# Kernel optimization log

Hardware: AMD Instinct MI355X
Metric: run time of the kernel (lower is better)

## Reference

```python
import jax, jax.numpy as jnp
import numpy as np

K, D, N, W, OUT = 16, 2, 16384, 256, 1
TW = 0.2  # fixed_transition_width


def setup_inputs() -> dict:
    key = jax.random.key(0)
    ks = jax.random.split(key, 9)
    # 4x4 grid of subdomains over [0,1]^2
    edges = np.linspace(0.0, 1.0, 5).astype(np.float32)
    mins = np.array([[edges[i], edges[j]] for i in range(4) for j in range(4)], np.float32)
    maxs = mins + 0.25

    def init_w(k, shape, fan_in):
        return jax.random.normal(k, shape, jnp.float32) / np.sqrt(fan_in).astype(np.float32)

    return {
        "x": jax.random.uniform(ks[0], (N, D), jnp.float32),
        "W0": init_w(ks[1], (K, D, W), D),
        "b0": jnp.zeros((K, W), jnp.float32),
        "W1": init_w(ks[2], (K, W, W), W),
        "b1": jnp.zeros((K, W), jnp.float32),
        "W2": init_w(ks[3], (K, W, W), W),
        "b2": jnp.zeros((K, W), jnp.float32),
        "W3": init_w(ks[4], (K, W, OUT), W),
        "b3": jnp.zeros((K, OUT), jnp.float32),
        "xmins": jnp.asarray(mins),
        "xmaxs": jnp.asarray(maxs),
    }


def _cosine_window(xmins, xmaxs, wmin, x):
    """Normalized cosine partition-of-unity weights. x:[N,D], xmins/xmaxs:[K,D] -> [N,K]."""
    # smooth ramp 0->1 over [xmin-w, xmin+w] and 1->0 over [xmax-w, xmax+w], per dim
    t_l = jnp.clip((x[None] - (xmins - wmin)[:, None]) / (2.0 * wmin), 0.0, 1.0)  # [K,N,D]
    t_r = jnp.clip(((xmaxs + wmin)[:, None] - x[None]) / (2.0 * wmin), 0.0, 1.0)
    w_raw = jnp.prod(0.25 * (1.0 - jnp.cos(jnp.pi * t_l)) * (1.0 - jnp.cos(jnp.pi * t_r)), axis=-1)  # [K,N]
    w = w_raw / (jnp.sum(w_raw, axis=0, keepdims=True) + 1e-9)
    return w.T  # [N,K]


def reference(x, W0, b0, W1, b1, W2, b2, W3, b3, xmins, xmaxs):
    all_w = _cosine_window(xmins, xmaxs, TW, x)  # [N,K]
    # per-subdomain normalization of x to [-1,1]
    center = (xmins + xmaxs) * 0.5
    scale = jnp.maximum((xmaxs - xmins) * 0.5, 1e-9)
    xn = (x[None] - center[:, None]) / scale[:, None]  # [K,N,D]
    # batched small MLPs (one per subdomain), tanh hidden activations
    h = jnp.tanh(jnp.einsum('knd,kdw->knw', xn, W0) + b0[:, None])
    h = jnp.tanh(jnp.einsum('knw,kwv->knv', h, W1) + b1[:, None])
    h = jnp.tanh(jnp.einsum('knw,kwv->knv', h, W2) + b2[:, None])
    sub = jnp.einsum('knw,kwo->kno', h, W3) + b3[:, None]  # [K,N,OUT]
    # window-weighted combine; ansatz is identity in the NN output
    return jnp.einsum('nk,kno->no', all_w, sub)  # [N,OUT]
```

## Files before the change

kernel.cpp:

```cpp
#include <hip/hip_runtime.h>
#include <stdint.h>

#define TWF 0.2f
#define NPTS 16384

typedef __attribute__((ext_vector_type(8))) short short8;
typedef __attribute__((ext_vector_type(4))) float floatx4;

__device__ __forceinline__ short f2bf(float f){
  unsigned u = __float_as_uint(f);
  u += 0x7fff + ((u >> 16) & 1);
  return (short)(u >> 16);
}
__device__ __forceinline__ float bf2f(short s){
  return __uint_as_float(((unsigned)(unsigned short)s) << 16);
}
__device__ __forceinline__ float fast_tanh(float x){
  float e = __builtin_amdgcn_exp2f(x * 2.885390082f);
  float r = __builtin_amdgcn_rcpf(e + 1.f);
  return fmaf(-2.f, r, 1.f);
}
__device__ __forceinline__ float cospi_t(float t){
  return __builtin_amdgcn_cosf(t * 0.5f);
}
__device__ __forceinline__ int swz(int m, int j){
  return m * 256 + ((((j >> 3) ^ (m & 7)) << 3) | (j & 7));
}

#define WS_W      0
#define WS_CNT    (4u<<20)
#define WS_ILIST  ((4u<<20) + 4096u)
#define WS_WLIST  ((5u<<20) + 4096u)
#define CNT(k)    counts[(k) * 32]

__global__ __launch_bounds__(256) void prep_fused(
    const float* __restrict__ W1, const float* __restrict__ W2,
    const float* __restrict__ x,  const float* __restrict__ xmins,
    const float* __restrict__ xmaxs, short* __restrict__ dst,
    int* __restrict__ counts, int* __restrict__ ilist, float* __restrict__ wlist,
    float* __restrict__ out){
  if (blockIdx.x < 1024){
    int gid = blockIdx.x * 256 + threadIdx.x;
    int lane = gid & 63; int rest = gid >> 6;
    int jt = rest & 15; rest >>= 4;
    int ks = rest & 7;  rest >>= 3;
    int k  = rest & 15; int mat = rest >> 4;
    const float* W = mat ? W2 : W1;
    int j   = jt * 16 + (lane & 15);
    int kk0 = ks * 32 + (lane >> 4) * 8;
    short8 v;
    #pragma unroll
    for (int jj = 0; jj < 8; jj++)
      v[jj] = f2bf(W[k * 65536 + (kk0 + jj) * 256 + j]);
    *(short8*)(dst + (size_t)gid * 8) = v;
  } else {
    __shared__ int s_wcnt[4];
    __shared__ int s_base;
    int gid  = (blockIdx.x - 1024) * 256 + threadIdx.x;
    int t    = threadIdx.x;
    int lane = t & 63, wave = t >> 6;
    out[gid] = 0.f;
    float px = x[gid * 2 + 0], py = x[gid * 2 + 1];
    float wr[16]; float sum = 0.f;
    #pragma unroll
    for (int k = 0; k < 16; k++){
      float w = 1.f;
      #pragma unroll
      for (int d = 0; d < 2; d++){
        float xv = d ? py : px;
        float mn = xmins[k * 2 + d], mx = xmaxs[k * 2 + d];
        float tl = fminf(fmaxf((xv - (mn - TWF)) * (1.f / (2.f * TWF)), 0.f), 1.f);
        float tr = fminf(fmaxf(((mx + TWF) - xv) * (1.f / (2.f * TWF)), 0.f), 1.f);
        w *= 0.25f * (1.f - cospi_t(tl)) * (1.f - cospi_t(tr));
      }
      wr[k] = w; sum += w;
    }
    float inv = 1.f / (sum + 1e-9f);
    #pragma unroll 1
    for (int kk = 0; kk < 16; kk++){
      int k = (kk + blockIdx.x) & 15;
      bool act = wr[k] > 0.f;
      unsigned long long mask = __ballot(act);
      if (lane == 0) s_wcnt[wave] = (int)__popcll(mask);
      __syncthreads();
      int tot = s_wcnt[0] + s_wcnt[1] + s_wcnt[2] + s_wcnt[3];
      int wpre = 0;
      #pragma unroll
      for (int w = 0; w < 4; w++) wpre += (w < wave) ? s_wcnt[w] : 0;
      if (t == 0) s_base = atomicAdd(&CNT(k), tot);
      __syncthreads();
      if (act){
        int pos = s_base + wpre + (int)__popcll(mask & ((1ull << lane) - 1ull));
        ilist[k * NPTS + pos] = gid;
        wlist[k * NPTS + pos] = wr[k] * inv;
      }
    }
  }
}

__global__ __launch_bounds__(256, 3) void fbpinn_main(
    const float* __restrict__ x,  const float* __restrict__ W0, const float* __restrict__ b0,
    const float* __restrict__ b1, const float* __restrict__ b2,
    const float* __restrict__ W3, const float* __restrict__ b3,
    const float* __restrict__ xmins, const float* __restrict__ xmaxs,
    const short* __restrict__ wsw, const int* __restrict__ counts,
    const int* __restrict__ ilist, const float* __restrict__ wlist,
    float* __restrict__ out)
{
  __shared__ short lds_h[64 * 256];
  __shared__ float s_xn[64 * 2];
  __shared__ float s_win[64];
  __shared__ int   s_pidx[64];
  __shared__ float s_w3[256];
  __shared__ float s_w0[512];

  const int t    = threadIdx.x;
  const int lane = t & 63;
  const int wave = t >> 6;
  const int col  = lane & 15;
  const int quad = lane >> 4;

  int tb[17]; tb[0] = 0;
  #pragma unroll
  for (int kk = 0; kk < 16; kk++) tb[kk + 1] = tb[kk] + ((CNT(kk) + 63) >> 6);
  const int total = tb[16];

  for (int tile = blockIdx.x; tile < total; tile += gridDim.x){
    int k = 0;
    #pragma unroll
    for (int kk = 1; kk < 16; kk++) k += (tile >= tb[kk]);
    const int base = (tile - tb[k]) * 64;
    const int cnt  = CNT(k);

    __syncthreads();

    s_w3[t] = W3[k * 256 + t];
    s_w0[t] = W0[k * 512 + t];
    s_w0[256 + t] = W0[k * 512 + 256 + t];
    if (t < 64){
      int gi = base + t;
      bool valid = gi < cnt;
      int pidx = valid ? ilist[k * NPTS + gi] : 0;
      float w  = valid ? wlist[k * NPTS + gi] : 0.f;
      s_pidx[t] = pidx;
      s_win[t]  = w;
      float px = x[pidx * 2 + 0], py = x[pidx * 2 + 1];
      float cx = (xmins[k * 2 + 0] + xmaxs[k * 2 + 0]) * 0.5f;
      float cy = (xmins[k * 2 + 1] + xmaxs[k * 2 + 1]) * 0.5f;
      float sx = fmaxf((xmaxs[k * 2 + 0] - xmins[k * 2 + 0]) * 0.5f, 1e-9f);
      float sy = fmaxf((xmaxs[k * 2 + 1] - xmins[k * 2 + 1]) * 0.5f, 1e-9f);
      s_xn[t * 2 + 0] = (px - cx) / sx;
      s_xn[t * 2 + 1] = (py - cy) / sy;
    }
    __syncthreads();

    {
      short8 bfr[4], afr[4];
      #pragma unroll
      for (int jtl = 0; jtl < 4; jtl++){
        int j = (wave * 4 + jtl) * 16 + col;
        short8 b;
        #pragma unroll
        for (int i = 0; i < 8; i++) b[i] = 0;
        b[0] = (quad == 0) ? f2bf(s_w0[j])       : (short)0;
        b[1] = (quad == 0) ? f2bf(s_w0[256 + j]) : (short)0;
        bfr[jtl] = b;
      }
      #pragma unroll
      for (int mt = 0; mt < 4; mt++){
        int m = mt * 16 + col;
        short8 a;
        #pragma unroll
        for (int i = 0; i < 8; i++) a[i] = 0;
        a[0] = (quad == 0) ? f2bf(s_xn[m * 2 + 0]) : (short)0;
        a[1] = (quad == 0) ? f2bf(s_xn[m * 2 + 1]) : (short)0;
        afr[mt] = a;
      }
      floatx4 acc[4][4];
      #pragma unroll
      for (int a = 0; a < 4; a++)
        #pragma unroll
        for (int b = 0; b < 4; b++)
          acc[a][b] = (floatx4){0.f, 0.f, 0.f, 0.f};
      #pragma unroll
      for (int mt = 0; mt < 4; mt++)
        #pragma unroll
        for (int jtl = 0; jtl < 4; jtl++)
          acc[mt][jtl] = __builtin_amdgcn_mfma_f32_16x16x32_bf16(afr[mt], bfr[jtl], acc[mt][jtl], 0, 0, 0);
      #pragma unroll
      for (int jtl = 0; jtl < 4; jtl++){
        int j = (wave * 4 + jtl) * 16 + col;
        float bb = b0[k * 256 + j];
        #pragma unroll
        for (int mt = 0; mt < 4; mt++){
          #pragma unroll
          for (int r = 0; r < 4; r++){
            int m = mt * 16 + quad * 4 + r;
            lds_h[swz(m, j)] = f2bf(fast_tanh(acc[mt][jtl][r] + bb));
          }
        }
      }
      __syncthreads();
    }

    #pragma unroll 1
    for (int layer = 0; layer < 2; layer++){
      const short8* wb = (const short8*)(wsw + (size_t)layer * 1048576)
                         + ((size_t)(k * 8) * 16 + wave * 4) * 64 + lane;
      const float*  bp = layer ? b2 : b1;
      floatx4 acc[4][4];
      #pragma unroll
      for (int a = 0; a < 4; a++)
        #pragma unroll
        for (int b = 0; b < 4; b++)
          acc[a][b] = (floatx4){0.f, 0.f, 0.f, 0.f};

      short8 bcur[4];
      #pragma unroll
      for (int jtl = 0; jtl < 4; jtl++) bcur[jtl] = wb[jtl * 64];

      #pragma unroll
      for (int ks = 0; ks < 8; ks++){
        short8 bnxt[4];
        if (ks < 7){
          #pragma unroll
          for (int jtl = 0; jtl < 4; jtl++)
            bnxt[jtl] = wb[(ks + 1) * 1024 + jtl * 64];
        }
        short8 afr[4];
        #pragma unroll
        for (int mt = 0; mt < 4; mt++){
          int m   = mt * 16 + col;
          int pos = (ks * 4 + quad) ^ (m & 7);
          afr[mt] = *(const short8*)&lds_h[m * 256 + pos * 8];
        }
        #pragma unroll
        for (int mt = 0; mt < 4; mt++)
          #pragma unroll
          for (int jtl = 0; jtl < 4; jtl++)
            acc[mt][jtl] = __builtin_amdgcn_mfma_f32_16x16x32_bf16(afr[mt], bcur[jtl], acc[mt][jtl], 0, 0, 0);
        if (ks < 7){
          #pragma unroll
          for (int jtl = 0; jtl < 4; jtl++) bcur[jtl] = bnxt[jtl];
        }
      }
      __syncthreads();

      #pragma unroll
      for (int jtl = 0; jtl < 4; jtl++){
        int j = (wave * 4 + jtl) * 16 + col;
        float bb = bp[k * 256 + j];
        #pragma unroll
        for (int mt = 0; mt < 4; mt++){
          #pragma unroll
          for (int r = 0; r < 4; r++){
            int m = mt * 16 + quad * 4 + r;
            lds_h[swz(m, j)] = f2bf(fast_tanh(acc[mt][jtl][r] + bb));
          }
        }
      }
      __syncthreads();
    }

    {
      int m = t >> 2, q = t & 3;
      float dot = 0.f;
      #pragma unroll
      for (int cc = 0; cc < 8; cc++){
        int ci  = q * 8 + cc;
        int pos = ci ^ (m & 7);
        short8 hv = *(const short8*)&lds_h[m * 256 + pos * 8];
        #pragma unroll
        for (int jj = 0; jj < 8; jj++)
          dot = fmaf(bf2f(hv[jj]), s_w3[ci * 8 + jj], dot);
      }
      dot += __shfl_xor(dot, 1);
      dot += __shfl_xor(dot, 2);
      if (q == 0 && s_win[m] != 0.f)
        atomicAdd(&out[s_pidx[m]], s_win[m] * (dot + b3[k]));
    }
  }
}

extern "C" void kernel_launch(void* const* d_in, const int* in_sizes, int n_in,
                              void* d_out, int out_size, void* d_ws, size_t ws_size,
                              hipStream_t stream){
  const float* x     = (const float*)d_in[0];
  const float* W0    = (const float*)d_in[1];
  const float* b0    = (const float*)d_in[2];
  const float* W1    = (const float*)d_in[3];
  const float* b1    = (const float*)d_in[4];
  const float* W2    = (const float*)d_in[5];
  const float* b2    = (const float*)d_in[6];
  const float* W3    = (const float*)d_in[7];
  const float* b3    = (const float*)d_in[8];
  const float* xmins = (const float*)d_in[9];
  const float* xmaxs = (const float*)d_in[10];
  float* out = (float*)d_out;

  char* ws = (char*)d_ws;
  short* wsw   = (short*)(ws + WS_W);
  int*   cnts  = (int*)  (ws + WS_CNT);
  int*   ilist = (int*)  (ws + WS_ILIST);
  float* wlist = (float*)(ws + WS_WLIST);

  (void)hipMemsetAsync(cnts, 0, 4096, stream);
  prep_fused<<<1024 + NPTS / 256, 256, 0, stream>>>(W1, W2, x, xmins, xmaxs,
                                                    wsw, cnts, ilist, wlist, out);
  fbpinn_main<<<640, 256, 0, stream>>>(x, W0, b0, b1, b2, W3, b3, xmins, xmaxs,
                                       wsw, cnts, ilist, wlist, out);
}
```

Baseline: 155.3 us.

## Replace global atomic compaction with per-wave segment counts and prefix-scan lookup

The binning step no longer uses block barriers and a global atomicAdd per subdomain. Each wave now writes its compacted points into a fixed 64-slot segment and records a byte count per segment. The main kernel rebuilds per-subdomain totals and each tile's gather indices from those counts with wave shuffle reductions, a prefix scan and a binary search. This also drops the memset launch, raises the occupancy hint to 4 and enlarges the main grid to 1024 blocks, at the cost of extra scan work in every tile.

```diff
diff --git a/kernel.cpp b/kernel.cpp
--- a/kernel.cpp
+++ b/kernel.cpp
@@ -31,14 +31,13 @@
 #define WS_CNT    (4u<<20)
 #define WS_ILIST  ((4u<<20) + 4096u)
 #define WS_WLIST  ((5u<<20) + 4096u)
-#define CNT(k)    counts[(k) * 32]
 
 __global__ __launch_bounds__(256) void prep_fused(
     const float* __restrict__ W1, const float* __restrict__ W2,
     const float* __restrict__ x,  const float* __restrict__ xmins,
     const float* __restrict__ xmaxs, short* __restrict__ dst,
-    int* __restrict__ counts, int* __restrict__ ilist, float* __restrict__ wlist,
-    float* __restrict__ out){
+    unsigned char* __restrict__ cnt8, int* __restrict__ ilist,
+    float* __restrict__ wlist, float* __restrict__ out){
   if (blockIdx.x < 1024){
     int gid = blockIdx.x * 256 + threadIdx.x;
     int lane = gid & 63; int rest = gid >> 6;
@@ -54,13 +53,13 @@
       v[jj] = f2bf(W[k * 65536 + (kk0 + jj) * 256 + j]);
     *(short8*)(dst + (size_t)gid * 8) = v;
   } else {
-    __shared__ int s_wcnt[4];
-    __shared__ int s_base;
-    int gid  = (blockIdx.x - 1024) * 256 + threadIdx.x;
+    int bb   = blockIdx.x - 1024;
     int t    = threadIdx.x;
     int lane = t & 63, wave = t >> 6;
-    out[gid] = 0.f;
-    float px = x[gid * 2 + 0], py = x[gid * 2 + 1];
+    out[bb * 256 + t] = 0.f;
+    int seg = bb * 4 + wave;
+    int pt  = seg * 64 + lane;
+    float px = x[pt * 2 + 0], py = x[pt * 2 + 1];
     float wr[16]; float sum = 0.f;
     #pragma unroll
     for (int k = 0; k < 16; k++){
@@ -77,33 +76,25 @@
     }
     float inv = 1.f / (sum + 1e-9f);
     #pragma unroll 1
-    for (int kk = 0; kk < 16; kk++){
-      int k = (kk + blockIdx.x) & 15;
+    for (int k = 0; k < 16; k++){
       bool act = wr[k] > 0.f;
       unsigned long long mask = __ballot(act);
-      if (lane == 0) s_wcnt[wave] = (int)__popcll(mask);
-      __syncthreads();
-      int tot = s_wcnt[0] + s_wcnt[1] + s_wcnt[2] + s_wcnt[3];
-      int wpre = 0;
-      #pragma unroll
-      for (int w = 0; w < 4; w++) wpre += (w < wave) ? s_wcnt[w] : 0;
-      if (t == 0) s_base = atomicAdd(&CNT(k), tot);
-      __syncthreads();
+      if (lane == 0) cnt8[k * 256 + seg] = (unsigned char)__popcll(mask);
       if (act){
-        int pos = s_base + wpre + (int)__popcll(mask & ((1ull << lane) - 1ull));
-        ilist[k * NPTS + pos] = gid;
-        wlist[k * NPTS + pos] = wr[k] * inv;
+        int pos = (int)__popcll(mask & ((1ull << lane) - 1ull));
+        ilist[k * NPTS + seg * 64 + pos] = pt;
+        wlist[k * NPTS + seg * 64 + pos] = wr[k] * inv;
       }
     }
   }
 }
 
-__global__ __launch_bounds__(256, 3) void fbpinn_main(
+__global__ __launch_bounds__(256, 4) void fbpinn_main(
     const float* __restrict__ x,  const float* __restrict__ W0, const float* __restrict__ b0,
     const float* __restrict__ b1, const float* __restrict__ b2,
     const float* __restrict__ W3, const float* __restrict__ b3,
     const float* __restrict__ xmins, const float* __restrict__ xmaxs,
-    const short* __restrict__ wsw, const int* __restrict__ counts,
+    const short* __restrict__ wsw, const unsigned int* __restrict__ cnt32,
     const int* __restrict__ ilist, const float* __restrict__ wlist,
     float* __restrict__ out)
 {
@@ -113,6 +104,7 @@
   __shared__ int   s_pidx[64];
   __shared__ float s_w3[256];
   __shared__ float s_w0[512];
+  __shared__ int   s_tot[16];
 
   const int t    = threadIdx.x;
   const int lane = t & 63;
@@ -120,9 +112,21 @@
   const int col  = lane & 15;
   const int quad = lane >> 4;
 
+  if (t < 64){
+    #pragma unroll
+    for (int k = 0; k < 16; k++){
+      unsigned p = cnt32[k * 64 + t];
+      int s4 = (int)((p & 255u) + ((p >> 8) & 255u) + ((p >> 16) & 255u) + (p >> 24));
+      #pragma unroll
+      for (int d = 1; d < 64; d <<= 1) s4 += __shfl_xor(s4, d);
+      if (t == 0) s_tot[k] = s4;
+    }
+  }
+  __syncthreads();
+
   int tb[17]; tb[0] = 0;
   #pragma unroll
-  for (int kk = 0; kk < 16; kk++) tb[kk + 1] = tb[kk] + ((CNT(kk) + 63) >> 6);
+  for (int kk = 0; kk < 16; kk++) tb[kk + 1] = tb[kk] + ((s_tot[kk] + 63) >> 6);
   const int total = tb[16];
 
   for (int tile = blockIdx.x; tile < total; tile += gridDim.x){
@@ -130,7 +134,7 @@
     #pragma unroll
     for (int kk = 1; kk < 16; kk++) k += (tile >= tb[kk]);
     const int base = (tile - tb[k]) * 64;
-    const int cnt  = CNT(k);
+    const int cnt  = s_tot[k];
 
     __syncthreads();
 
@@ -138,10 +142,36 @@
     s_w0[t] = W0[k * 512 + t];
     s_w0[256 + t] = W0[k * 512 + 256 + t];
     if (t < 64){
-      int gi = base + t;
-      bool valid = gi < cnt;
-      int pidx = valid ? ilist[k * NPTS + gi] : 0;
-      float w  = valid ? wlist[k * NPTS + gi] : 0.f;
+      unsigned pack = cnt32[k * 64 + t];
+      int s4 = (int)((pack & 255u) + ((pack >> 8) & 255u) + ((pack >> 16) & 255u) + (pack >> 24));
+      int inc = s4;
+      #pragma unroll
+      for (int d = 1; d < 64; d <<= 1){
+        int v = __shfl_up(inc, d);
+        if (t >= d) inc += v;
+      }
+      int excl = inc - s4;
+      int g = base + t;
+      bool valid = g < cnt;
+      int gg = valid ? g : 0;
+      int lo = 0;
+      #pragma unroll
+      for (int d = 32; d >= 1; d >>= 1){
+        int cand = lo + d;
+        int e = __shfl(excl, cand & 63);
+        if (cand < 64 && e <= gg) lo = cand;
+      }
+      int e_lo = __shfl(excl, lo);
+      unsigned p_lo = (unsigned)__shfl((int)pack, lo);
+      int rem = gg - e_lo;
+      int b0v = (int)(p_lo & 255u), b1v = (int)((p_lo >> 8) & 255u), b2v = (int)((p_lo >> 16) & 255u);
+      int r = 0;
+      if (rem >= b0v){ rem -= b0v; r = 1;
+        if (rem >= b1v){ rem -= b1v; r = 2;
+          if (rem >= b2v){ rem -= b2v; r = 3; } } }
+      int idx = k * NPTS + (lo * 4 + r) * 64 + rem;
+      int pidx = valid ? ilist[idx] : 0;
+      float w  = valid ? wlist[idx] : 0.f;
       s_pidx[t] = pidx;
       s_win[t]  = w;
       float px = x[pidx * 2 + 0], py = x[pidx * 2 + 1];
@@ -299,14 +329,14 @@
   float* out = (float*)d_out;
 
   char* ws = (char*)d_ws;
-  short* wsw   = (short*)(ws + WS_W);
-  int*   cnts  = (int*)  (ws + WS_CNT);
-  int*   ilist = (int*)  (ws + WS_ILIST);
-  float* wlist = (float*)(ws + WS_WLIST);
-
-  (void)hipMemsetAsync(cnts, 0, 4096, stream);
-  prep_fused<<<1024 + NPTS / 256, 256, 0, stream>>>(W1, W2, x, xmins, xmaxs,
-                                                    wsw, cnts, ilist, wlist, out);
-  fbpinn_main<<<640, 256, 0, stream>>>(x, W0, b0, b1, b2, W3, b3, xmins, xmaxs,
-                                       wsw, cnts, ilist, wlist, out);
-}
+  short*         wsw   = (short*)        (ws + WS_W);
+  unsigned char* cnt8  = (unsigned char*)(ws + WS_CNT);
+  int*           ilist = (int*)          (ws + WS_ILIST);
+  float*         wlist = (float*)        (ws + WS_WLIST);
+
+  prep_fused<<<1088, 256, 0, stream>>>(W1, W2, x, xmins, xmaxs,
+                                       wsw, cnt8, ilist, wlist, out);
+  fbpinn_main<<<1024, 256, 0, stream>>>(x, W0, b0, b1, b2, W3, b3, xmins, xmaxs,
+                                        wsw, (const unsigned int*)cnt8,
+                                        ilist, wlist, out);
+}
```

New measurement: 175.3 us. 12.9% more time.
